# Optimization experiments

Measured on AMD Instinct MI355X. Metric: run time of the kernel, lower is better.

The kernel has to match this reference:

```python
import jax, jax.numpy as jnp
import numpy as np

B, C_IN, T = 8, 1024, 8192
K, D = 1024, 8  # codebook_size, codebook_dim


def setup_inputs() -> dict:
    key = jax.random.key(0)
    ks = jax.random.split(key, 6)
    z = jax.random.normal(ks[0], (B, C_IN, T), dtype=jnp.float32)
    # effective (post weight-norm) 1x1 conv weights, kernel dim squeezed
    in_w = jax.random.normal(ks[1], (D, C_IN), dtype=jnp.float32) * (1.0 / np.sqrt(C_IN))
    in_b = jax.random.normal(ks[2], (D,), dtype=jnp.float32) * 0.01
    codebook = jax.random.normal(ks[3], (K, D), dtype=jnp.float32)
    out_w = jax.random.normal(ks[4], (C_IN, D), dtype=jnp.float32) * (1.0 / np.sqrt(D))
    out_b = jax.random.normal(ks[5], (C_IN,), dtype=jnp.float32) * 0.01
    return {"z": z, "in_w": in_w, "in_b": in_b, "codebook": codebook,
            "out_w": out_w, "out_b": out_b}


def reference(z, in_w, in_b, codebook, out_w, out_b):
    # in_proj: 1x1 Conv1d over channels  [B,C,T] -> [B,D,T]
    z_e = jnp.einsum('bct,dc->bdt', z, in_w) + in_b[None, :, None]
    enc = z_e.transpose(0, 2, 1).reshape(-1, z_e.shape[1])  # [B*T, D]
    # squared-L2 distance to every codebook entry: ||e||^2 - 2 e.w + ||w||^2
    dist = ((enc * enc).sum(1, keepdims=True)
            - 2.0 * enc @ codebook.T
            + (codebook * codebook).sum(1)[None, :])  # [B*T, K]
    ids = jnp.argmax(-dist, axis=1).reshape(z.shape[0], -1)  # [B, T]
    # decode: embedding gather + 1x1 out_proj  [B,T,D] -> [B,C,T]
    z_q = codebook[ids]  # [B, T, D]
    out = jnp.einsum('btd,cd->bct', z_q, out_w) + out_b[None, :, None]
    return out, ids
```

## Files before the change

### kernel.cpp

```cpp
#include <hip/hip_runtime.h>

#define B_   8
#define C_   1024
#define T_   8192
#define K_   1024
#define D_   8
#define CT_  (C_ * T_)
#define BT_  (B_ * T_)
#define OUTN_ ((size_t)B_ * CT_)

__global__ __launch_bounds__(256) void vq_prep(
    const float* __restrict__ in_w, const float* __restrict__ in_b,
    const float* __restrict__ cb, float* __restrict__ wT,
    float* __restrict__ nrm)
{
    const int i = blockIdx.x * 256 + threadIdx.x;
    if (i < C_ * D_) {
        const int d = i >> 10;
        const int c = i & (C_ - 1);
        wT[c * D_ + d] = in_w[i];
    }
    if (i < K_) {
        float s = 0.0f, q = 0.0f;
#pragma unroll
        for (int d = 0; d < D_; ++d) {
            const float w = cb[i * D_ + d];
            s = fmaf(w, w, s);
            q = fmaf(in_b[d], w, q);
        }
        nrm[i] = 0.5f * s - q;
    }
}

__global__ __launch_bounds__(256, 4) void vq_fused(
    const float* __restrict__ z, const float* __restrict__ wT,
    const float* __restrict__ nrm, const float* __restrict__ cb,
    const float* __restrict__ out_w, const float* __restrict__ out_b,
    float* __restrict__ out, float* __restrict__ ids_f)
{
    __shared__ float s_p[2048];

    const int tid = threadIdx.x;
    const int wu  = __builtin_amdgcn_readfirstlane(tid >> 6);
    const int l   = tid & 63;
    const int bt0 = blockIdx.x * 64;
    const int b   = bt0 >> 13;
    const int t0  = bt0 & (T_ - 1);
    const int c0  = wu * 256;

    float acc[D_];
#pragma unroll
    for (int d = 0; d < D_; ++d) acc[d] = 0.0f;

    const float* zp = z + (size_t)b * CT_ + (size_t)c0 * T_ + (t0 + l);
    for (int i0 = 0; i0 < 256; i0 += 16) {
        float zv[16];
#pragma unroll
        for (int u = 0; u < 16; ++u) zv[u] = zp[(size_t)(i0 + u) * T_];
#pragma unroll
        for (int u = 0; u < 16; ++u) {
            const float* wr = wT + (size_t)(c0 + i0 + u) * D_;
#pragma unroll
            for (int d = 0; d < D_; ++d) acc[d] = fmaf(zv[u], wr[d], acc[d]);
        }
    }
#pragma unroll
    for (int d = 0; d < D_; ++d) s_p[wu * 512 + d * 64 + l] = acc[d];
    __syncthreads();

    for (int p = tid; p < 512; p += 256)
        s_p[p] = s_p[p] + s_p[512 + p] + s_p[1024 + p] + s_p[1536 + p];
    __syncthreads();

    float e[D_];
#pragma unroll
    for (int d = 0; d < D_; ++d) e[d] = s_p[d * 64 + l];

    float best = 3.4e38f;
    int   bi   = 0;
    for (int j = 0; j < 256; ++j) {
        const int k = c0 + j;
        const float* cr = cb + (size_t)k * D_;
        float s = nrm[k];
#pragma unroll
        for (int d = 0; d < D_; ++d) s = fmaf(-e[d], cr[d], s);
        if (s < best) { best = s; bi = k; }
    }
    s_p[1024 + wu * 64 + l] = best;
    ((int*)s_p)[1280 + wu * 64 + l] = bi;
    __syncthreads();

    if (tid < 64) {
        float bv = s_p[1024 + l];
        int   bb = ((int*)s_p)[1280 + l];
#pragma unroll
        for (int ww = 1; ww < 4; ++ww) {
            const float v = s_p[1024 + ww * 64 + l];
            if (v < bv) { bv = v; bb = ((int*)s_p)[1280 + ww * 64 + l]; }
        }
        ids_f[bt0 + l] = (float)bb;
        const float4* cp = (const float4*)(cb + (size_t)bb * D_);
        const float4 a = cp[0], q = cp[1];
        float* zq = s_p + l * D_;
        zq[0] = a.x; zq[1] = a.y; zq[2] = a.z; zq[3] = a.w;
        zq[4] = q.x; zq[5] = q.y; zq[6] = q.z; zq[7] = q.w;
    }
    __syncthreads();

    float r[D_];
#pragma unroll
    for (int d = 0; d < D_; ++d) r[d] = s_p[l * D_ + d];

    float* op = out + (size_t)b * CT_ + (size_t)c0 * T_ + (t0 + l);
#pragma unroll 8
    for (int j = 0; j < 256; ++j) {
        const int c = c0 + j;
        const float* wr = out_w + (size_t)c * D_;
        float o = out_b[c];
#pragma unroll
        for (int d = 0; d < D_; ++d) o = fmaf(r[d], wr[d], o);
        op[(size_t)j * T_] = o;
    }
}

extern "C" void kernel_launch(void* const* d_in, const int* in_sizes, int n_in,
                              void* d_out, int out_size, void* d_ws, size_t ws_size,
                              hipStream_t stream) {
    const float* z    = (const float*)d_in[0];
    const float* in_w = (const float*)d_in[1];
    const float* in_b = (const float*)d_in[2];
    const float* cb   = (const float*)d_in[3];
    const float* ow   = (const float*)d_in[4];
    const float* ob   = (const float*)d_in[5];

    float* out   = (float*)d_out;
    float* ids_f = out + OUTN_;

    float* wT  = (float*)d_ws;
    float* nrm = wT + C_ * D_;

    vq_prep<<<32, 256, 0, stream>>>(in_w, in_b, cb, wT, nrm);
    vq_fused<<<BT_ / 64, 256, 0, stream>>>(z, wT, nrm, cb, ow, ob, out, ids_f);
}
```

Measured before the change: 523.8 us.

## Widen fused VQ blocks to 256 timesteps with float4 vectorized loads and stores

Each block now covers 256 timesteps with 1024 threads (16 waves), and every lane handles 4 consecutive timesteps through float4 loads of z and float4 stores of out. Each wave reduces 64 channels and scans 64 codebook entries. Partial sums and argmin candidates are combined through a larger padded shared-memory buffer. The goal is wider memory transactions and reuse of each weight/codebook scalar across 4 timesteps, at the cost of a 256-block grid that uses about 150KB of LDS per block, which limits occupancy to one block per CU.

```diff
diff --git a/kernel.cpp b/kernel.cpp
--- a/kernel.cpp
+++ b/kernel.cpp
@@ -32,94 +32,144 @@
     }
 }
 
-__global__ __launch_bounds__(256, 4) void vq_fused(
+__global__ __launch_bounds__(1024, 4) void vq_fused(
     const float* __restrict__ z, const float* __restrict__ wT,
     const float* __restrict__ nrm, const float* __restrict__ cb,
     const float* __restrict__ out_w, const float* __restrict__ out_b,
     float* __restrict__ out, float* __restrict__ ids_f)
 {
-    __shared__ float s_p[2048];
+    __shared__ float s_part[32 * 1025];
+    __shared__ float s_enc[2048];
+    __shared__ float s_zq[256 * 9];
+
+    float* s_val = s_part;
+    int*   s_idx = (int*)(s_part + 4096);
 
     const int tid = threadIdx.x;
     const int wu  = __builtin_amdgcn_readfirstlane(tid >> 6);
     const int l   = tid & 63;
-    const int bt0 = blockIdx.x * 64;
-    const int b   = bt0 >> 13;
-    const int t0  = bt0 & (T_ - 1);
-    const int c0  = wu * 256;
+    const int blk = blockIdx.x;
+    const int b   = blk >> 5;
+    const int t0  = (blk & 31) << 8;
+    const int c0  = wu << 6;
 
-    float acc[D_];
+    float acc[4][D_];
 #pragma unroll
-    for (int d = 0; d < D_; ++d) acc[d] = 0.0f;
+    for (int tt = 0; tt < 4; ++tt)
+#pragma unroll
+        for (int d = 0; d < D_; ++d) acc[tt][d] = 0.0f;
 
-    const float* zp = z + (size_t)b * CT_ + (size_t)c0 * T_ + (t0 + l);
-    for (int i0 = 0; i0 < 256; i0 += 16) {
-        float zv[16];
+    const float4* zp =
+        (const float4*)(z + (size_t)b * CT_ + (size_t)c0 * T_ + t0) + l;
+    for (int i = 0; i < 64; i += 4) {
+        float4 zv[4];
 #pragma unroll
-        for (int u = 0; u < 16; ++u) zv[u] = zp[(size_t)(i0 + u) * T_];
+        for (int u = 0; u < 4; ++u)
+            zv[u] = zp[(size_t)(i + u) * (T_ / 4)];
 #pragma unroll
-        for (int u = 0; u < 16; ++u) {
-            const float* wr = wT + (size_t)(c0 + i0 + u) * D_;
+        for (int u = 0; u < 4; ++u) {
+            const float* wr = wT + (size_t)(c0 + i + u) * D_;
 #pragma unroll
-            for (int d = 0; d < D_; ++d) acc[d] = fmaf(zv[u], wr[d], acc[d]);
+            for (int d = 0; d < D_; ++d) {
+                const float wv = wr[d];
+                acc[0][d] = fmaf(zv[u].x, wv, acc[0][d]);
+                acc[1][d] = fmaf(zv[u].y, wv, acc[1][d]);
+                acc[2][d] = fmaf(zv[u].z, wv, acc[2][d]);
+                acc[3][d] = fmaf(zv[u].w, wv, acc[3][d]);
+            }
         }
     }
 #pragma unroll
-    for (int d = 0; d < D_; ++d) s_p[wu * 512 + d * 64 + l] = acc[d];
+    for (int tt = 0; tt < 4; ++tt)
+#pragma unroll
+        for (int d = 0; d < D_; ++d)
+            s_part[(tt * D_ + d) * 1025 + tid] = acc[tt][d];
     __syncthreads();
 
-    for (int p = tid; p < 512; p += 256)
-        s_p[p] = s_p[p] + s_p[512 + p] + s_p[1024 + p] + s_p[1536 + p];
-    __syncthreads();
-
-    float e[D_];
 #pragma unroll
-    for (int d = 0; d < D_; ++d) e[d] = s_p[d * 64 + l];
-
-    float best = 3.4e38f;
-    int   bi   = 0;
-    for (int j = 0; j < 256; ++j) {
-        const int k = c0 + j;
-        const float* cr = cb + (size_t)k * D_;
-        float s = nrm[k];
+    for (int r = 0; r < 2; ++r) {
+        const int p = tid + r * 1024;
+        const int k = p >> 6, l2 = p & 63;
+        float s = 0.0f;
 #pragma unroll
-        for (int d = 0; d < D_; ++d) s = fmaf(-e[d], cr[d], s);
-        if (s < best) { best = s; bi = k; }
-    }
-    s_p[1024 + wu * 64 + l] = best;
-    ((int*)s_p)[1280 + wu * 64 + l] = bi;
-    __syncthreads();
-
-    if (tid < 64) {
-        float bv = s_p[1024 + l];
-        int   bb = ((int*)s_p)[1280 + l];
-#pragma unroll
-        for (int ww = 1; ww < 4; ++ww) {
-            const float v = s_p[1024 + ww * 64 + l];
-            if (v < bv) { bv = v; bb = ((int*)s_p)[1280 + ww * 64 + l]; }
-        }
-        ids_f[bt0 + l] = (float)bb;
-        const float4* cp = (const float4*)(cb + (size_t)bb * D_);
-        const float4 a = cp[0], q = cp[1];
-        float* zq = s_p + l * D_;
-        zq[0] = a.x; zq[1] = a.y; zq[2] = a.z; zq[3] = a.w;
-        zq[4] = q.x; zq[5] = q.y; zq[6] = q.z; zq[7] = q.w;
+        for (int ww = 0; ww < 16; ++ww)
+            s += s_part[k * 1025 + ww * 64 + l2];
+        s_enc[p] = s;
     }
     __syncthreads();
 
-    float r[D_];
+    float e[4][D_];
 #pragma unroll
-    for (int d = 0; d < D_; ++d) r[d] = s_p[l * D_ + d];
+    for (int tt = 0; tt < 4; ++tt)
+#pragma unroll
+        for (int d = 0; d < D_; ++d)
+            e[tt][d] = s_enc[(tt * D_ + d) * 64 + l];
 
-    float* op = out + (size_t)b * CT_ + (size_t)c0 * T_ + (t0 + l);
-#pragma unroll 8
-    for (int j = 0; j < 256; ++j) {
+    float best[4];
+    int   bi[4];
+#pragma unroll
+    for (int tt = 0; tt < 4; ++tt) { best[tt] = 3.4e38f; bi[tt] = 0; }
+
+    for (int j = 0; j < 64; ++j) {
+        const int k = c0 + j;
+        const float* cr = cb + (size_t)k * D_;
+        const float nk = nrm[k];
+#pragma unroll
+        for (int tt = 0; tt < 4; ++tt) {
+            float s = nk;
+#pragma unroll
+            for (int d = 0; d < D_; ++d) s = fmaf(-e[tt][d], cr[d], s);
+            if (s < best[tt]) { best[tt] = s; bi[tt] = k; }
+        }
+    }
+#pragma unroll
+    for (int tt = 0; tt < 4; ++tt) {
+        s_val[wu * 256 + 4 * l + tt] = best[tt];
+        s_idx[wu * 256 + 4 * l + tt] = bi[tt];
+    }
+    __syncthreads();
+
+    if (tid < 256) {
+        float bv = s_val[tid];
+        int   bb = s_idx[tid];
+#pragma unroll
+        for (int ww = 1; ww < 16; ++ww) {
+            const float v = s_val[ww * 256 + tid];
+            if (v < bv) { bv = v; bb = s_idx[ww * 256 + tid]; }
+        }
+        ids_f[blk * 256 + tid] = (float)bb;
+        const float4* cp = (const float4*)(cb + (size_t)bb * D_);
+        const float4 a = cp[0], q = cp[1];
+        float* zr = s_zq + tid * 9;
+        zr[0] = a.x; zr[1] = a.y; zr[2] = a.z; zr[3] = a.w;
+        zr[4] = q.x; zr[5] = q.y; zr[6] = q.z; zr[7] = q.w;
+    }
+    __syncthreads();
+
+    float r4[4][D_];
+#pragma unroll
+    for (int tt = 0; tt < 4; ++tt)
+#pragma unroll
+        for (int d = 0; d < D_; ++d)
+            r4[tt][d] = s_zq[(4 * l + tt) * 9 + d];
+
+    float4* op = (float4*)(out + (size_t)b * CT_ + (size_t)c0 * T_ + t0) + l;
+#pragma unroll 4
+    for (int j = 0; j < 64; ++j) {
         const int c = c0 + j;
         const float* wr = out_w + (size_t)c * D_;
-        float o = out_b[c];
+        const float bias = out_b[c];
+        float4 o;
+        o.x = bias; o.y = bias; o.z = bias; o.w = bias;
 #pragma unroll
-        for (int d = 0; d < D_; ++d) o = fmaf(r[d], wr[d], o);
-        op[(size_t)j * T_] = o;
+        for (int d = 0; d < D_; ++d) {
+            const float wv = wr[d];
+            o.x = fmaf(r4[0][d], wv, o.x);
+            o.y = fmaf(r4[1][d], wv, o.y);
+            o.z = fmaf(r4[2][d], wv, o.z);
+            o.w = fmaf(r4[3][d], wv, o.w);
+        }
+        op[(size_t)j * (T_ / 4)] = o;
     }
 }
 
@@ -140,5 +190,5 @@
     float* nrm = wT + C_ * D_;
 
     vq_prep<<<32, 256, 0, stream>>>(in_w, in_b, cb, wT, nrm);
-    vq_fused<<<BT_ / 64, 256, 0, stream>>>(z, wT, nrm, cb, ow, ob, out, ids_f);
+    vq_fused<<<256, 1024, 0, stream>>>(z, wT, nrm, cb, ow, ob, out, ids_f);
 }
```

Result: faster. 468.6 us (-10.5%).
